# Kernel tuning notes

Measured on AMD Instinct MI355X. Metric: run time of the kernel, lower is better.

The kernel has to match this reference:

```python
import jax, jax.numpy as jnp
import numpy as np

N, E, CIN, H, B, NCOV, NCLASS, T = 50000, 800000, 64, 64, 256, 8, 2, 3


def setup_inputs() -> dict:
    key = jax.random.key(0)
    ks = jax.random.split(key, 24)
    s = 1.0 / np.sqrt(H)
    nrm = lambda k, shp, sc: (jax.random.normal(k, shp, jnp.float32) * sc)
    p = {}
    p["x"] = nrm(ks[0], (N, 3 * CIN), 1.0)
    p["edge_index"] = jax.random.randint(ks[1], (2, E), 0, N)
    p["cov"] = nrm(ks[2], (B, NCOV), 1.0)
    p["batch"] = jnp.sort(jax.random.randint(ks[3], (N,), 0, B))
    p["h0"] = nrm(ks[4], (B, H), 1.0)
    p["c0"] = nrm(ks[5], (B, H), 1.0)
    # GCNEncoder params (shared across the 3 channel slices, as in the torch code)
    p["lin_W"] = nrm(ks[6], (CIN, H), s)
    p["lin_b"] = jnp.zeros((H,), jnp.float32)
    p["conv1_W"] = nrm(ks[7], (H, H), s)
    p["conv1_b"] = jnp.zeros((H,), jnp.float32)
    p["conv2_W"] = nrm(ks[8], (H, H), s)
    p["conv2_b"] = jnp.zeros((H,), jnp.float32)
    # LSTM (1 layer), torch gate order i,f,g,o
    p["Wih"] = nrm(ks[9], (4 * H, H), s)
    p["Whh"] = nrm(ks[10], (4 * H, H), s)
    p["bih"] = jnp.zeros((4 * H,), jnp.float32)
    p["bhh"] = jnp.zeros((4 * H,), jnp.float32)
    p["w0_W"] = nrm(ks[11], (H, H), s)
    p["w0_b"] = jnp.zeros((H,), jnp.float32)
    p["attn_W"] = nrm(ks[12], (1, H), s)
    p["attn_b"] = jnp.zeros((1,), jnp.float32)
    p["l1_W"] = nrm(ks[13], (8, H), s)
    p["l1_b"] = jnp.zeros((8,), jnp.float32)
    p["l2_W"] = nrm(ks[14], (NCLASS, 8 + NCOV), 1.0 / np.sqrt(8 + NCOV))
    p["l2_b"] = jnp.zeros((NCLASS,), jnp.float32)
    return p


def _gcn_conv(x, src, dst, dinv, W, b):
    xw = x @ W
    norm = dinv[src] * dinv[dst]                      # [E]
    agg = jax.ops.segment_sum(norm[:, None] * xw[src], dst, num_segments=N)
    agg = agg + (2.0 * dinv * dinv)[:, None] * xw     # self-loop (weight 2)
    return agg + b


def _encoder(x, src, dst, dinv, lin_W, lin_b, c1W, c1b, c2W, c2b):
    out = x @ lin_W + lin_b                           # dropout = identity (eval)
    out1 = jax.nn.relu(_gcn_conv(out, src, dst, dinv, c1W, c1b)) + out
    out2 = _gcn_conv(out1, src, dst, dinv, c2W, c2b) + out1
    return out2


def reference(x, edge_index, cov, batch, h0, c0, lin_W, lin_b, conv1_W, conv1_b,
              conv2_W, conv2_b, Wih, Whh, bih, bhh, w0_W, w0_b, attn_W, attn_b,
              l1_W, l1_b, l2_W, l2_b):
    src, dst = edge_index[0], edge_index[1]
    deg = jax.ops.segment_sum(jnp.ones((E,), jnp.float32), dst, num_segments=N) + 2.0
    dinv = jax.lax.rsqrt(deg)
    enc = lambda xi: _encoder(xi, src, dst, dinv, lin_W, lin_b,
                              conv1_W, conv1_b, conv2_W, conv2_b)
    o1 = enc(x[:, :CIN]); o2 = enc(x[:, CIN:2 * CIN]); o3 = enc(x[:, 2 * CIN:])
    # global_mean_pool per branch
    cnt = jnp.maximum(jax.ops.segment_sum(jnp.ones((N,), jnp.float32), batch,
                                          num_segments=B), 1.0)[:, None]
    pool = lambda o: jax.ops.segment_sum(o, batch, num_segments=B) / cnt
    seq = jnp.stack([pool(o1), pool(o2), pool(o3)], axis=1)  # [B, 3, H]

    # 1-layer LSTM over T=3 (torch gate order i,f,g,o)
    def step(carry, x_t):
        h, c = carry
        g = x_t @ Wih.T + bih + h @ Whh.T + bhh
        i, f, gg, o = jnp.split(g, 4, axis=-1)
        c = jax.nn.sigmoid(f) * c + jax.nn.sigmoid(i) * jnp.tanh(gg)
        h = jax.nn.sigmoid(o) * jnp.tanh(c)
        return (h, c), h

    (_, _), hs = jax.lax.scan(step, (h0, c0), jnp.swapaxes(seq, 0, 1))
    rnn_out = jnp.swapaxes(hs, 0, 1)                         # [B, T, H]
    r = jnp.tanh(rnn_out @ w0_W.T + w0_b)
    attn = jax.nn.softmax((r @ attn_W.T + attn_b)[..., 0], axis=1)  # [B, T]
    pooled = jnp.einsum('bth,bt->bh', r, attn)
    out = jax.nn.relu(pooled @ l1_W.T + l1_b)
    out = jnp.concatenate([out, cov], axis=1)
    out = out @ l2_W.T + l2_b
    return attn, out
```

## Files before the change

kernel.cpp:

```cpp
#include <hip/hip_runtime.h>
#include <math.h>


#define TT 3
#define CHUNK 2048

typedef __attribute__((ext_vector_type(2))) float floatx2;

__device__ __forceinline__ float sigmoidf_(float x) { return 1.f / (1.f + expf(-x)); }

__global__ void brow_sorted(const int* __restrict__ batch, int* __restrict__ brow,
                            int N, int B) {
    int n = blockIdx.x * 256 + threadIdx.x;
    if (n >= N) return;
    int b = batch[n];
    if (n == 0) {
        for (int q = 0; q <= b; ++q) brow[q] = 0;
    } else {
        int pb = batch[n - 1];
        for (int q = pb + 1; q <= b; ++q) brow[q] = n;
    }
    if (n == N - 1) {
        for (int q = b + 1; q <= B; ++q) brow[q] = N;
    }
}

__global__ void hist_kernel(const int* __restrict__ dst, int* __restrict__ bcnt, int E) {
    __shared__ int h[256];
    h[threadIdx.x] = 0;
    __syncthreads();
    int base = blockIdx.x * CHUNK;
    for (int i = threadIdx.x; i < CHUNK; i += 256) {
        int e = base + i;
        if (e < E) atomicAdd(&h[dst[e] >> 8], 1);
    }
    __syncthreads();
    int v = h[threadIdx.x];
    if (v) atomicAdd(&bcnt[threadIdx.x], v);
}

__global__ void scan_buckets(const int* __restrict__ bcnt, int* __restrict__ boff,
                             int* __restrict__ bcur, int nb, int E) {
    __shared__ int s[256];
    int v = (threadIdx.x < nb) ? bcnt[threadIdx.x] : 0;
    s[threadIdx.x] = v;
    __syncthreads();
    for (int off = 1; off < 256; off <<= 1) {
        int t = (threadIdx.x >= off) ? s[threadIdx.x - off] : 0;
        __syncthreads();
        s[threadIdx.x] += t;
        __syncthreads();
    }
    if (threadIdx.x < nb) { boff[threadIdx.x] = s[threadIdx.x] - v; bcur[threadIdx.x] = s[threadIdx.x] - v; }
    if (threadIdx.x == 0) boff[nb] = E;
}

__global__ void stage_kernel(const int* __restrict__ src, const int* __restrict__ dst,
                             int* __restrict__ bcur, unsigned* __restrict__ stg, int E) {
    __shared__ int hcnt[256], hbase[256], hcur[256];
    hcnt[threadIdx.x] = 0;
    __syncthreads();
    int base = blockIdx.x * CHUNK;
    for (int i = threadIdx.x; i < CHUNK; i += 256) {
        int e = base + i;
        if (e < E) atomicAdd(&hcnt[dst[e] >> 8], 1);
    }
    __syncthreads();
    int c = hcnt[threadIdx.x];
    if (c) hbase[threadIdx.x] = atomicAdd(&bcur[threadIdx.x], c);
    hcur[threadIdx.x] = 0;
    __syncthreads();
    for (int i = threadIdx.x; i < CHUNK; i += 256) {
        int e = base + i;
        if (e < E) {
            int d = dst[e];
            int b = d >> 8;
            int r = atomicAdd(&hcur[b], 1);
            stg[hbase[b] + r] = (unsigned)src[e] | ((unsigned)(d & 255) << 24);
        }
    }
}

__global__ void bucket_build(const unsigned* __restrict__ stg, const int* __restrict__ boff,
                             int* __restrict__ rowptr, float* __restrict__ dinv,
                             int* __restrict__ csrc, int N, int E) {
    const int b = blockIdx.x;
    const int n0 = b << 8;
    __shared__ int cnt[256];
    __shared__ int pfx[256];
    cnt[threadIdx.x] = 0;
    __syncthreads();
    const int s = boff[b], e = boff[b + 1];
    for (int p = s + threadIdx.x; p < e; p += 256)
        atomicAdd(&cnt[stg[p] >> 24], 1);
    __syncthreads();
    int v = cnt[threadIdx.x];
    pfx[threadIdx.x] = v;
    __syncthreads();
    for (int off = 1; off < 256; off <<= 1) {
        int t = (threadIdx.x >= off) ? pfx[threadIdx.x - off] : 0;
        __syncthreads();
        pfx[threadIdx.x] += t;
        __syncthreads();
    }
    int rowbase = s + pfx[threadIdx.x] - v;
    int n = n0 + threadIdx.x;
    if (n < N) {
        rowptr[n] = rowbase;
        dinv[n] = rsqrtf((float)v + 2.0f);
    }
    if (b == 0 && threadIdx.x == 0) rowptr[N] = E;
    cnt[threadIdx.x] = rowbase;
    __syncthreads();
    for (int p = s + threadIdx.x; p < e; p += 256) {
        unsigned u = stg[p];
        int dl = u >> 24;
        int r = atomicAdd(&cnt[dl], 1);
        csrc[r] = (int)(u & 0xFFFFFFu);
    }
}

__global__ __launch_bounds__(256) void gemm64_v2(
    const float* __restrict__ A, int lda, long aStride,
    const float* __restrict__ W, const float* __restrict__ bias,
    float* __restrict__ C, long cStride,
    unsigned* __restrict__ T8, const float* __restrict__ dinvp, int nrows) {
    __shared__ float AT[64][68];
    __shared__ float Ws[64][68];
    const int t = threadIdx.x;
    const float* Ab = A + (long)blockIdx.y * aStride;
    const int r0 = blockIdx.x * 64;

    #pragma unroll
    for (int i = 0; i < 4; ++i) {
        int idx = t + i * 256;
        int k = idx >> 4, c4 = idx & 15;
        float4 w = *(const float4*)(W + k * 64 + c4 * 4);
        *(float4*)&Ws[k][c4 * 4] = w;
    }
    #pragma unroll
    for (int i = 0; i < 4; ++i) {
        int idx = t + i * 256;
        int row = idx >> 4, c4 = idx & 15;
        int gr = r0 + row;
        float4 a = make_float4(0.f, 0.f, 0.f, 0.f);
        if (gr < nrows) a = *(const float4*)(Ab + (long)gr * lda + c4 * 4);
        AT[c4 * 4 + 0][row] = a.x;
        AT[c4 * 4 + 1][row] = a.y;
        AT[c4 * 4 + 2][row] = a.z;
        AT[c4 * 4 + 3][row] = a.w;
    }
    __syncthreads();

    const int rowg = t >> 4;
    const int colg = t & 15;
    float acc[4][4] = {};
    #pragma unroll 8
    for (int k = 0; k < 64; ++k) {
        float4 av = *(const float4*)&AT[k][rowg * 4];
        float4 wv = *(const float4*)&Ws[k][colg * 4];
        acc[0][0] = fmaf(av.x, wv.x, acc[0][0]);
        acc[0][1] = fmaf(av.x, wv.y, acc[0][1]);
        acc[0][2] = fmaf(av.x, wv.z, acc[0][2]);
        acc[0][3] = fmaf(av.x, wv.w, acc[0][3]);
        acc[1][0] = fmaf(av.y, wv.x, acc[1][0]);
        acc[1][1] = fmaf(av.y, wv.y, acc[1][1]);
        acc[1][2] = fmaf(av.y, wv.z, acc[1][2]);
        acc[1][3] = fmaf(av.y, wv.w, acc[1][3]);
        acc[2][0] = fmaf(av.z, wv.x, acc[2][0]);
        acc[2][1] = fmaf(av.z, wv.y, acc[2][1]);
        acc[2][2] = fmaf(av.z, wv.z, acc[2][2]);
        acc[2][3] = fmaf(av.z, wv.w, acc[2][3]);
        acc[3][0] = fmaf(av.w, wv.x, acc[3][0]);
        acc[3][1] = fmaf(av.w, wv.y, acc[3][1]);
        acc[3][2] = fmaf(av.w, wv.z, acc[3][2]);
        acc[3][3] = fmaf(av.w, wv.w, acc[3][3]);
    }

    float b0 = bias ? bias[colg * 4 + 0] : 0.f;
    float b1 = bias ? bias[colg * 4 + 1] : 0.f;
    float b2 = bias ? bias[colg * 4 + 2] : 0.f;
    float b3 = bias ? bias[colg * 4 + 3] : 0.f;
    #pragma unroll
    for (int i = 0; i < 4; ++i) {
        int gr = r0 + rowg * 4 + i;
        if (gr >= nrows) continue;
        float c0 = acc[i][0] + b0, c1 = acc[i][1] + b1;
        float c2 = acc[i][2] + b2, c3 = acc[i][3] + b3;
        if (C) {
            float* Cb = C + (long)blockIdx.y * cStride;
            *(float4*)(Cb + (long)gr * 64 + colg * 4) = make_float4(c0, c1, c2, c3);
        }
        if (T8) {
            float sc = dinvp[gr];
            int r = 0;
            r = __builtin_amdgcn_cvt_pk_fp8_f32(c0 * sc, c1 * sc, r, false);
            r = __builtin_amdgcn_cvt_pk_fp8_f32(c2 * sc, c3 * sc, r, true);
            T8[(long)gr * 48 + blockIdx.y * 16 + colg] = (unsigned)r;
        }
    }
}

template <bool RELU>
__global__ __launch_bounds__(256) void gcn_gather3_f8(
    const int* __restrict__ rowptr, const int* __restrict__ csrc,
    const float* __restrict__ dinv, const unsigned* __restrict__ tc,
    const float* __restrict__ bias, const float* __restrict__ prev, long chS,
    float* __restrict__ outp, int N) {
    long gid = ((long)blockIdx.x * 256 + threadIdx.x) >> 4;
    int n = (int)gid;
    if (n >= N) return;
    const int jj = threadIdx.x & 15;

    const int end = rowptr[n + 1];
    const float din = dinv[n];
    float a0[TT] = {}, a1[TT] = {}, a2[TT] = {}, a3[TT] = {};
    int p = rowptr[n];
    for (; p + 3 < end; p += 4) {
        long r0 = (long)csrc[p] * 48 + jj;
        long r1 = (long)csrc[p + 1] * 48 + jj;
        long r2 = (long)csrc[p + 2] * 48 + jj;
        long r3 = (long)csrc[p + 3] * 48 + jj;
        #pragma unroll
        for (int ch = 0; ch < TT; ++ch) {
            unsigned u0 = tc[r0 + ch * 16];
            unsigned u1 = tc[r1 + ch * 16];
            unsigned u2 = tc[r2 + ch * 16];
            unsigned u3 = tc[r3 + ch * 16];
            floatx2 l0 = __builtin_amdgcn_cvt_pk_f32_fp8(u0, false);
            floatx2 h0 = __builtin_amdgcn_cvt_pk_f32_fp8(u0, true);
            floatx2 l1 = __builtin_amdgcn_cvt_pk_f32_fp8(u1, false);
            floatx2 h1 = __builtin_amdgcn_cvt_pk_f32_fp8(u1, true);
            floatx2 l2 = __builtin_amdgcn_cvt_pk_f32_fp8(u2, false);
            floatx2 h2 = __builtin_amdgcn_cvt_pk_f32_fp8(u2, true);
            floatx2 l3 = __builtin_amdgcn_cvt_pk_f32_fp8(u3, false);
            floatx2 h3 = __builtin_amdgcn_cvt_pk_f32_fp8(u3, true);
            a0[ch] += (l0.x + l1.x) + (l2.x + l3.x);
            a1[ch] += (l0.y + l1.y) + (l2.y + l3.y);
            a2[ch] += (h0.x + h1.x) + (h2.x + h3.x);
            a3[ch] += (h0.y + h1.y) + (h2.y + h3.y);
        }
    }
    for (; p < end; ++p) {
        long r = (long)csrc[p] * 48 + jj;
        #pragma unroll
        for (int ch = 0; ch < TT; ++ch) {
            unsigned u = tc[r + ch * 16];
            floatx2 lo = __builtin_amdgcn_cvt_pk_f32_fp8(u, false);
            floatx2 hi = __builtin_amdgcn_cvt_pk_f32_fp8(u, true);
            a0[ch] += lo.x; a1[ch] += lo.y; a2[ch] += hi.x; a3[ch] += hi.y;
        }
    }
    float4 bv = *(const float4*)(bias + 4 * jj);
    long nrow = (long)n * 48 + jj;
    long off = (long)n * 64 + 4 * jj;
    #pragma unroll
    for (int ch = 0; ch < TT; ++ch) {
        unsigned us = tc[nrow + ch * 16];
        floatx2 slo = __builtin_amdgcn_cvt_pk_f32_fp8(us, false);
        floatx2 shi = __builtin_amdgcn_cvt_pk_f32_fp8(us, true);
        float v0 = (a0[ch] + 2.f * slo.x) * din + bv.x;
        float v1 = (a1[ch] + 2.f * slo.y) * din + bv.y;
        float v2 = (a2[ch] + 2.f * shi.x) * din + bv.z;
        float v3 = (a3[ch] + 2.f * shi.y) * din + bv.w;
        if (RELU) {
            v0 = fmaxf(v0, 0.f); v1 = fmaxf(v1, 0.f);
            v2 = fmaxf(v2, 0.f); v3 = fmaxf(v3, 0.f);
        }
        float4 pv = *(const float4*)(prev + ch * chS + off);
        *(float4*)(outp + ch * chS + off) =
            make_float4(v0 + pv.x, v1 + pv.y, v2 + pv.z, v3 + pv.w);
    }
}

__global__ __launch_bounds__(256) void pool_range(
    const float* __restrict__ out2, long chStride, const int* __restrict__ brow,
    float* __restrict__ seq) {
    const int b = blockIdx.x;
    const int chan = blockIdx.y;
    const float* src = out2 + (long)chan * chStride;
    const int j = threadIdx.x & 63;
    const int w = threadIdx.x >> 6;
    __shared__ float part[4][64];
    float acc = 0.f;
    const int s = brow[b], e = brow[b + 1];
    for (int n = s + w; n < e; n += 4) acc += src[(long)n * 64 + j];
    part[w][j] = acc;
    __syncthreads();
    if (w == 0)
        seq[((long)b * TT + chan) * 64 + j] = part[0][j] + part[1][j] + part[2][j] + part[3][j];
}

__global__ __launch_bounds__(256) void head_kernel(
    const float* __restrict__ seq, const int* __restrict__ brow,
    const float* __restrict__ h0, const float* __restrict__ c0,
    const float* __restrict__ Wih, const float* __restrict__ Whh,
    const float* __restrict__ bih, const float* __restrict__ bhh,
    const float* __restrict__ w0W, const float* __restrict__ w0b,
    const float* __restrict__ attnW, const float* __restrict__ attnb,
    const float* __restrict__ l1W, const float* __restrict__ l1b,
    const float* __restrict__ l2W, const float* __restrict__ l2b,
    const float* __restrict__ cov, float* __restrict__ out_attn,
    float* __restrict__ out_cls) {
    const int b = blockIdx.x;
    const int t = threadIdx.x;

    __shared__ float x[TT][64];
    __shared__ float h[64], c[64];
    __shared__ float gates[256];
    __shared__ float rnn[TT][64];
    __shared__ float r[TT][64];
    __shared__ float logit[TT];
    __shared__ float a[TT];
    __shared__ float pooled[64];
    __shared__ float l1o[16];

    float inv = 1.0f / fmaxf((float)(brow[b + 1] - brow[b]), 1.0f);
    if (t < TT * 64) x[t / 64][t % 64] = seq[(long)b * TT * 64 + t] * inv;
    if (t < 64) { h[t] = h0[(long)b * 64 + t]; c[t] = c0[(long)b * 64 + t]; }
    __syncthreads();

    for (int step = 0; step < TT; ++step) {
        float g = bih[t] + bhh[t];
        const float* wi = Wih + (long)t * 64;
        const float* wh = Whh + (long)t * 64;
        #pragma unroll 8
        for (int k = 0; k < 64; ++k) g += wi[k] * x[step][k] + wh[k] * h[k];
        gates[t] = g;
        __syncthreads();
        if (t < 64) {
            float ig = sigmoidf_(gates[t]);
            float fg = sigmoidf_(gates[64 + t]);
            float gg = tanhf(gates[128 + t]);
            float og = sigmoidf_(gates[192 + t]);
            float cn = fg * c[t] + ig * gg;
            c[t] = cn;
            float hn = og * tanhf(cn);
            h[t] = hn;
            rnn[step][t] = hn;
        }
        __syncthreads();
    }

    if (t < TT * 64) {
        int tt = t / 64, j = t % 64;
        float v = w0b[j];
        const float* wr = w0W + (long)j * 64;
        #pragma unroll 8
        for (int k = 0; k < 64; ++k) v += rnn[tt][k] * wr[k];
        r[tt][j] = tanhf(v);
    }
    __syncthreads();

    if (t < TT) {
        float v = attnb[0];
        #pragma unroll 8
        for (int k = 0; k < 64; ++k) v += r[t][k] * attnW[k];
        logit[t] = v;
    }
    __syncthreads();

    if (t == 0) {
        float m = fmaxf(logit[0], fmaxf(logit[1], logit[2]));
        float e0 = expf(logit[0] - m), e1 = expf(logit[1] - m), e2 = expf(logit[2] - m);
        float s = e0 + e1 + e2;
        a[0] = e0 / s; a[1] = e1 / s; a[2] = e2 / s;
        out_attn[(long)b * TT + 0] = a[0];
        out_attn[(long)b * TT + 1] = a[1];
        out_attn[(long)b * TT + 2] = a[2];
    }
    __syncthreads();

    if (t < 64) pooled[t] = a[0] * r[0][t] + a[1] * r[1][t] + a[2] * r[2][t];
    __syncthreads();

    if (t < 8) {
        float v = l1b[t];
        const float* w = l1W + (long)t * 64;
        #pragma unroll 8
        for (int k = 0; k < 64; ++k) v += pooled[k] * w[k];
        l1o[t] = fmaxf(v, 0.f);
    } else if (t < 16) {
        l1o[t] = cov[(long)b * 8 + (t - 8)];
    }
    __syncthreads();

    if (t < 2) {
        float v = l2b[t];
        const float* w = l2W + (long)t * 16;
        #pragma unroll
        for (int k = 0; k < 16; ++k) v += l1o[k] * w[k];
        out_cls[(long)b * 2 + t] = v;
    }
}

extern "C" void kernel_launch(void* const* d_in, const int* in_sizes, int n_in,
                              void* d_out, int out_size, void* d_ws, size_t ws_size,
                              hipStream_t stream) {
    const float* x       = (const float*)d_in[0];
    const int*   eidx    = (const int*)d_in[1];
    const float* cov     = (const float*)d_in[2];
    const int*   batch   = (const int*)d_in[3];
    const float* h0      = (const float*)d_in[4];
    const float* c0      = (const float*)d_in[5];
    const float* lin_W   = (const float*)d_in[6];
    const float* lin_b   = (const float*)d_in[7];
    const float* conv1_W = (const float*)d_in[8];
    const float* conv1_b = (const float*)d_in[9];
    const float* conv2_W = (const float*)d_in[10];
    const float* conv2_b = (const float*)d_in[11];
    const float* Wih     = (const float*)d_in[12];
    const float* Whh     = (const float*)d_in[13];
    const float* bih     = (const float*)d_in[14];
    const float* bhh     = (const float*)d_in[15];
    const float* w0_W    = (const float*)d_in[16];
    const float* w0_b    = (const float*)d_in[17];
    const float* attn_W  = (const float*)d_in[18];
    const float* attn_b  = (const float*)d_in[19];
    const float* l1_W    = (const float*)d_in[20];
    const float* l1_b    = (const float*)d_in[21];
    const float* l2_W    = (const float*)d_in[22];
    const float* l2_b    = (const float*)d_in[23];

    const int N = in_sizes[3];
    const int E = in_sizes[1] / 2;
    const int B = in_sizes[2] / 8;

    const int* src = eidx;
    const int* dst = eidx + E;

    auto cdiv = [](long a, long b) { return (int)((a + b - 1) / b); };
    const int nb = cdiv(N, 256);

    char* w = (char*)d_ws;
    float* dinv   = (float*)w;  w += (size_t)N * 4;
    int*   rowptr = (int*)w;    w += (size_t)(N + 1) * 4;
    int*   brow   = (int*)w;    w += (size_t)(B + 1) * 4;
    int*   bcnt   = (int*)w;    w += 256 * 4;
    int*   boff   = (int*)w;    w += 260 * 4;
    int*   bcur   = (int*)w;    w += 256 * 4;
    int*   csrc   = (int*)w;    w += (size_t)E * 4;
    unsigned* stg = (unsigned*)w; w += (size_t)E * 4;
    float* seq    = (float*)w;  w += (size_t)B * TT * 64 * 4;
    float* buf0   = (float*)w;  w += (size_t)TT * N * 64 * 4;
    float* bufA   = (float*)w;  w += (size_t)TT * N * 64 * 4;
    unsigned* tb8 = (unsigned*)w;  w += (size_t)N * 48 * 4;
    const long chS = (long)N * 64;

    float* out_attn = (float*)d_out;
    float* out_cls  = out_attn + (long)B * TT;

    hipMemsetAsync(bcnt, 0, 256 * 4, stream);
    brow_sorted<<<cdiv(N, 256), 256, 0, stream>>>(batch, brow, N, B);
    hist_kernel<<<cdiv(E, CHUNK), 256, 0, stream>>>(dst, bcnt, E);
    scan_buckets<<<1, 256, 0, stream>>>(bcnt, boff, bcur, nb, E);
    stage_kernel<<<cdiv(E, CHUNK), 256, 0, stream>>>(src, dst, bcur, stg, E);
    bucket_build<<<nb, 256, 0, stream>>>(stg, boff, rowptr, dinv, csrc, N, E);

    const int gemm_gx = cdiv(N, 64);
    const int ng_gx   = cdiv((long)N * 16, 256);

    {
        dim3 ggrid(gemm_gx, TT);
        gemm64_v2<<<ggrid, 256, 0, stream>>>(x, 3 * 64, 64, lin_W, lin_b,
                                             buf0, chS, nullptr, nullptr, N);
    }
    {
        dim3 ggrid(gemm_gx, TT);
        gemm64_v2<<<ggrid, 256, 0, stream>>>(buf0, 64, chS, conv1_W, nullptr,
                                             nullptr, 0, tb8, dinv, N);
    }
    gcn_gather3_f8<true><<<ng_gx, 256, 0, stream>>>(
        rowptr, csrc, dinv, tb8, conv1_b, buf0, chS, bufA, N);
    {
        dim3 ggrid(gemm_gx, TT);
        gemm64_v2<<<ggrid, 256, 0, stream>>>(bufA, 64, chS, conv2_W, nullptr,
                                             nullptr, 0, tb8, dinv, N);
    }
    gcn_gather3_f8<false><<<ng_gx, 256, 0, stream>>>(
        rowptr, csrc, dinv, tb8, conv2_b, bufA, chS, buf0, N);

    {
        dim3 pgrid(B, TT);
        pool_range<<<pgrid, 256, 0, stream>>>(buf0, chS, brow, seq);
    }

    head_kernel<<<B, 256, 0, stream>>>(seq, brow, h0, c0, Wih, Whh, bih, bhh,
                                       w0_W, w0_b, attn_W, attn_b, l1_W, l1_b,
                                       l2_W, l2_b, cov, out_attn, out_cls);
}
```

Baseline: 256.0 us.

## Fuse lin and conv1 GEMMs, drop histogram pass, unroll gather by eight

Fuses the input linear layer and the conv1 GEMM into one kernel that keeps the intermediate tile in shared memory. The fused kernel still writes buf0 for the residual path and no longer re-reads it for the second GEMM. The CSR build drops its separate histogram pass by staging edges into fixed-capacity per-bucket slots (BCAP) and scanning the counts afterwards. This assumes no bucket of 256 destination nodes holds more than 16384 edges. The gather loop is unrolled to eight edges per iteration to raise memory-level parallelism, at some register cost.

```diff
diff --git a/kernel.cpp b/kernel.cpp
--- a/kernel.cpp
+++ b/kernel.cpp
@@ -4,6 +4,7 @@
 
 #define TT 3
 #define CHUNK 2048
+#define BCAP 16384
 
 typedef __attribute__((ext_vector_type(2))) float floatx2;
 
@@ -25,38 +26,8 @@
     }
 }
 
-__global__ void hist_kernel(const int* __restrict__ dst, int* __restrict__ bcnt, int E) {
-    __shared__ int h[256];
-    h[threadIdx.x] = 0;
-    __syncthreads();
-    int base = blockIdx.x * CHUNK;
-    for (int i = threadIdx.x; i < CHUNK; i += 256) {
-        int e = base + i;
-        if (e < E) atomicAdd(&h[dst[e] >> 8], 1);
-    }
-    __syncthreads();
-    int v = h[threadIdx.x];
-    if (v) atomicAdd(&bcnt[threadIdx.x], v);
-}
-
-__global__ void scan_buckets(const int* __restrict__ bcnt, int* __restrict__ boff,
-                             int* __restrict__ bcur, int nb, int E) {
-    __shared__ int s[256];
-    int v = (threadIdx.x < nb) ? bcnt[threadIdx.x] : 0;
-    s[threadIdx.x] = v;
-    __syncthreads();
-    for (int off = 1; off < 256; off <<= 1) {
-        int t = (threadIdx.x >= off) ? s[threadIdx.x - off] : 0;
-        __syncthreads();
-        s[threadIdx.x] += t;
-        __syncthreads();
-    }
-    if (threadIdx.x < nb) { boff[threadIdx.x] = s[threadIdx.x] - v; bcur[threadIdx.x] = s[threadIdx.x] - v; }
-    if (threadIdx.x == 0) boff[nb] = E;
-}
-
-__global__ void stage_kernel(const int* __restrict__ src, const int* __restrict__ dst,
-                             int* __restrict__ bcur, unsigned* __restrict__ stg, int E) {
+__global__ void stage_direct(const int* __restrict__ src, const int* __restrict__ dst,
+                             int* __restrict__ bcnt, unsigned* __restrict__ stg, int E) {
     __shared__ int hcnt[256], hbase[256], hcur[256];
     hcnt[threadIdx.x] = 0;
     __syncthreads();
@@ -67,7 +38,7 @@
     }
     __syncthreads();
     int c = hcnt[threadIdx.x];
-    if (c) hbase[threadIdx.x] = atomicAdd(&bcur[threadIdx.x], c);
+    if (c) hbase[threadIdx.x] = atomicAdd(&bcnt[threadIdx.x], c);
     hcur[threadIdx.x] = 0;
     __syncthreads();
     for (int i = threadIdx.x; i < CHUNK; i += 256) {
@@ -76,22 +47,41 @@
             int d = dst[e];
             int b = d >> 8;
             int r = atomicAdd(&hcur[b], 1);
-            stg[hbase[b] + r] = (unsigned)src[e] | ((unsigned)(d & 255) << 24);
-        }
-    }
-}
-
-__global__ void bucket_build(const unsigned* __restrict__ stg, const int* __restrict__ boff,
-                             int* __restrict__ rowptr, float* __restrict__ dinv,
-                             int* __restrict__ csrc, int N, int E) {
+            stg[(long)b * BCAP + hbase[b] + r] =
+                (unsigned)src[e] | ((unsigned)(d & 255) << 24);
+        }
+    }
+}
+
+__global__ void scan_buckets(const int* __restrict__ bcnt, int* __restrict__ boff,
+                             int nb, int E) {
+    __shared__ int s[256];
+    int v = (threadIdx.x < nb) ? bcnt[threadIdx.x] : 0;
+    s[threadIdx.x] = v;
+    __syncthreads();
+    for (int off = 1; off < 256; off <<= 1) {
+        int t = (threadIdx.x >= off) ? s[threadIdx.x - off] : 0;
+        __syncthreads();
+        s[threadIdx.x] += t;
+        __syncthreads();
+    }
+    if (threadIdx.x < nb) boff[threadIdx.x] = s[threadIdx.x] - v;
+    if (threadIdx.x == 0) boff[nb] = E;
+}
+
+__global__ void bucket_build(const unsigned* __restrict__ stg, const int* __restrict__ bcnt,
+                             const int* __restrict__ boff, int* __restrict__ rowptr,
+                             float* __restrict__ dinv, int* __restrict__ csrc,
+                             int N, int E) {
     const int b = blockIdx.x;
     const int n0 = b << 8;
     __shared__ int cnt[256];
     __shared__ int pfx[256];
     cnt[threadIdx.x] = 0;
     __syncthreads();
-    const int s = boff[b], e = boff[b + 1];
-    for (int p = s + threadIdx.x; p < e; p += 256)
+    const long s = (long)b * BCAP;
+    const long e = s + bcnt[b];
+    for (long p = s + threadIdx.x; p < e; p += 256)
         atomicAdd(&cnt[stg[p] >> 24], 1);
     __syncthreads();
     int v = cnt[threadIdx.x];
@@ -103,7 +93,7 @@
         pfx[threadIdx.x] += t;
         __syncthreads();
     }
-    int rowbase = s + pfx[threadIdx.x] - v;
+    int rowbase = boff[b] + pfx[threadIdx.x] - v;
     int n = n0 + threadIdx.x;
     if (n < N) {
         rowptr[n] = rowbase;
@@ -112,7 +102,7 @@
     if (b == 0 && threadIdx.x == 0) rowptr[N] = E;
     cnt[threadIdx.x] = rowbase;
     __syncthreads();
-    for (int p = s + threadIdx.x; p < e; p += 256) {
+    for (long p = s + threadIdx.x; p < e; p += 256) {
         unsigned u = stg[p];
         int dl = u >> 24;
         int r = atomicAdd(&cnt[dl], 1);
@@ -120,10 +110,102 @@
     }
 }
 
-__global__ __launch_bounds__(256) void gemm64_v2(
-    const float* __restrict__ A, int lda, long aStride,
-    const float* __restrict__ W, const float* __restrict__ bias,
-    float* __restrict__ C, long cStride,
+__global__ __launch_bounds__(256) void gemm_lin_conv1(
+    const float* __restrict__ x, const float* __restrict__ W1,
+    const float* __restrict__ b1, const float* __restrict__ W2,
+    float* __restrict__ buf0, long chS,
+    unsigned* __restrict__ T8, const float* __restrict__ dinvp, int nrows) {
+    __shared__ float AT[64][68];
+    __shared__ float Ws[64][68];
+    const int t = threadIdx.x;
+    const int r0 = blockIdx.x * 64;
+    const int rowg = t >> 4, colg = t & 15;
+
+    #pragma unroll
+    for (int i = 0; i < 4; ++i) {
+        int idx = t + i * 256;
+        int k = idx >> 4, c4 = idx & 15;
+        *(float4*)&Ws[k][c4 * 4] = *(const float4*)(W1 + k * 64 + c4 * 4);
+    }
+    #pragma unroll
+    for (int i = 0; i < 4; ++i) {
+        int idx = t + i * 256;
+        int row = idx >> 4, c4 = idx & 15;
+        int gr = r0 + row;
+        float4 a = make_float4(0.f, 0.f, 0.f, 0.f);
+        if (gr < nrows) a = *(const float4*)(x + (long)gr * 192 + blockIdx.y * 64 + c4 * 4);
+        AT[c4 * 4 + 0][row] = a.x;
+        AT[c4 * 4 + 1][row] = a.y;
+        AT[c4 * 4 + 2][row] = a.z;
+        AT[c4 * 4 + 3][row] = a.w;
+    }
+    __syncthreads();
+
+    float acc[4][4] = {};
+    #pragma unroll 8
+    for (int k = 0; k < 64; ++k) {
+        float4 av = *(const float4*)&AT[k][rowg * 4];
+        float4 wv = *(const float4*)&Ws[k][colg * 4];
+        #pragma unroll
+        for (int i = 0; i < 4; ++i) {
+            acc[i][0] = fmaf(((const float*)&av)[i], wv.x, acc[i][0]);
+            acc[i][1] = fmaf(((const float*)&av)[i], wv.y, acc[i][1]);
+            acc[i][2] = fmaf(((const float*)&av)[i], wv.z, acc[i][2]);
+            acc[i][3] = fmaf(((const float*)&av)[i], wv.w, acc[i][3]);
+        }
+    }
+    float b_0 = b1[colg * 4 + 0], b_1 = b1[colg * 4 + 1];
+    float b_2 = b1[colg * 4 + 2], b_3 = b1[colg * 4 + 3];
+    __syncthreads();
+    float* buf0c = buf0 + (long)blockIdx.y * chS;
+    #pragma unroll
+    for (int i = 0; i < 4; ++i) {
+        int gr = r0 + rowg * 4 + i;
+        float c0 = acc[i][0] + b_0, c1 = acc[i][1] + b_1;
+        float c2 = acc[i][2] + b_2, c3 = acc[i][3] + b_3;
+        if (gr < nrows)
+            *(float4*)(buf0c + (long)gr * 64 + colg * 4) = make_float4(c0, c1, c2, c3);
+        int row = rowg * 4 + i;
+        AT[colg * 4 + 0][row] = c0;
+        AT[colg * 4 + 1][row] = c1;
+        AT[colg * 4 + 2][row] = c2;
+        AT[colg * 4 + 3][row] = c3;
+    }
+    #pragma unroll
+    for (int i = 0; i < 4; ++i) {
+        int idx = t + i * 256;
+        int k = idx >> 4, c4 = idx & 15;
+        *(float4*)&Ws[k][c4 * 4] = *(const float4*)(W2 + k * 64 + c4 * 4);
+    }
+    __syncthreads();
+
+    float acc2[4][4] = {};
+    #pragma unroll 8
+    for (int k = 0; k < 64; ++k) {
+        float4 av = *(const float4*)&AT[k][rowg * 4];
+        float4 wv = *(const float4*)&Ws[k][colg * 4];
+        #pragma unroll
+        for (int i = 0; i < 4; ++i) {
+            acc2[i][0] = fmaf(((const float*)&av)[i], wv.x, acc2[i][0]);
+            acc2[i][1] = fmaf(((const float*)&av)[i], wv.y, acc2[i][1]);
+            acc2[i][2] = fmaf(((const float*)&av)[i], wv.z, acc2[i][2]);
+            acc2[i][3] = fmaf(((const float*)&av)[i], wv.w, acc2[i][3]);
+        }
+    }
+    #pragma unroll
+    for (int i = 0; i < 4; ++i) {
+        int gr = r0 + rowg * 4 + i;
+        if (gr >= nrows) continue;
+        float sc = dinvp[gr];
+        int r = 0;
+        r = __builtin_amdgcn_cvt_pk_fp8_f32(acc2[i][0] * sc, acc2[i][1] * sc, r, false);
+        r = __builtin_amdgcn_cvt_pk_fp8_f32(acc2[i][2] * sc, acc2[i][3] * sc, r, true);
+        T8[(long)gr * 48 + blockIdx.y * 16 + colg] = (unsigned)r;
+    }
+}
+
+__global__ __launch_bounds__(256) void gemm64_t8(
+    const float* __restrict__ A, long aStride, const float* __restrict__ W,
     unsigned* __restrict__ T8, const float* __restrict__ dinvp, int nrows) {
     __shared__ float AT[64][68];
     __shared__ float Ws[64][68];
@@ -135,8 +217,7 @@
     for (int i = 0; i < 4; ++i) {
         int idx = t + i * 256;
         int k = idx >> 4, c4 = idx & 15;
-        float4 w = *(const float4*)(W + k * 64 + c4 * 4);
-        *(float4*)&Ws[k][c4 * 4] = w;
+        *(float4*)&Ws[k][c4 * 4] = *(const float4*)(W + k * 64 + c4 * 4);
     }
     #pragma unroll
     for (int i = 0; i < 4; ++i) {
@@ -144,7 +225,7 @@
         int row = idx >> 4, c4 = idx & 15;
         int gr = r0 + row;
         float4 a = make_float4(0.f, 0.f, 0.f, 0.f);
-        if (gr < nrows) a = *(const float4*)(Ab + (long)gr * lda + c4 * 4);
+        if (gr < nrows) a = *(const float4*)(Ab + (long)gr * 64 + c4 * 4);
         AT[c4 * 4 + 0][row] = a.x;
         AT[c4 * 4 + 1][row] = a.y;
         AT[c4 * 4 + 2][row] = a.z;
@@ -152,54 +233,38 @@
     }
     __syncthreads();
 
-    const int rowg = t >> 4;
-    const int colg = t & 15;
+    const int rowg = t >> 4, colg = t & 15;
     float acc[4][4] = {};
     #pragma unroll 8
     for (int k = 0; k < 64; ++k) {
         float4 av = *(const float4*)&AT[k][rowg * 4];
         float4 wv = *(const float4*)&Ws[k][colg * 4];
-        acc[0][0] = fmaf(av.x, wv.x, acc[0][0]);
-        acc[0][1] = fmaf(av.x, wv.y, acc[0][1]);
-        acc[0][2] = fmaf(av.x, wv.z, acc[0][2]);
-        acc[0][3] = fmaf(av.x, wv.w, acc[0][3]);
-        acc[1][0] = fmaf(av.y, wv.x, acc[1][0]);
-        acc[1][1] = fmaf(av.y, wv.y, acc[1][1]);
-        acc[1][2] = fmaf(av.y, wv.z, acc[1][2]);
-        acc[1][3] = fmaf(av.y, wv.w, acc[1][3]);
-        acc[2][0] = fmaf(av.z, wv.x, acc[2][0]);
-        acc[2][1] = fmaf(av.z, wv.y, acc[2][1]);
-        acc[2][2] = fmaf(av.z, wv.z, acc[2][2]);
-        acc[2][3] = fmaf(av.z, wv.w, acc[2][3]);
-        acc[3][0] = fmaf(av.w, wv.x, acc[3][0]);
-        acc[3][1] = fmaf(av.w, wv.y, acc[3][1]);
-        acc[3][2] = fmaf(av.w, wv.z, acc[3][2]);
-        acc[3][3] = fmaf(av.w, wv.w, acc[3][3]);
-    }
-
-    float b0 = bias ? bias[colg * 4 + 0] : 0.f;
-    float b1 = bias ? bias[colg * 4 + 1] : 0.f;
-    float b2 = bias ? bias[colg * 4 + 2] : 0.f;
-    float b3 = bias ? bias[colg * 4 + 3] : 0.f;
+        #pragma unroll
+        for (int i = 0; i < 4; ++i) {
+            acc[i][0] = fmaf(((const float*)&av)[i], wv.x, acc[i][0]);
+            acc[i][1] = fmaf(((const float*)&av)[i], wv.y, acc[i][1]);
+            acc[i][2] = fmaf(((const float*)&av)[i], wv.z, acc[i][2]);
+            acc[i][3] = fmaf(((const float*)&av)[i], wv.w, acc[i][3]);
+        }
+    }
     #pragma unroll
     for (int i = 0; i < 4; ++i) {
         int gr = r0 + rowg * 4 + i;
         if (gr >= nrows) continue;
-        float c0 = acc[i][0] + b0, c1 = acc[i][1] + b1;
-        float c2 = acc[i][2] + b2, c3 = acc[i][3] + b3;
-        if (C) {
-            float* Cb = C + (long)blockIdx.y * cStride;
-            *(float4*)(Cb + (long)gr * 64 + colg * 4) = make_float4(c0, c1, c2, c3);
-        }
-        if (T8) {
-            float sc = dinvp[gr];
-            int r = 0;
-            r = __builtin_amdgcn_cvt_pk_fp8_f32(c0 * sc, c1 * sc, r, false);
-            r = __builtin_amdgcn_cvt_pk_fp8_f32(c2 * sc, c3 * sc, r, true);
-            T8[(long)gr * 48 + blockIdx.y * 16 + colg] = (unsigned)r;
-        }
-    }
-}
+        float sc = dinvp[gr];
+        int r = 0;
+        r = __builtin_amdgcn_cvt_pk_fp8_f32(acc[i][0] * sc, acc[i][1] * sc, r, false);
+        r = __builtin_amdgcn_cvt_pk_fp8_f32(acc[i][2] * sc, acc[i][3] * sc, r, true);
+        T8[(long)gr * 48 + blockIdx.y * 16 + colg] = (unsigned)r;
+    }
+}
+
+#define EDGE3(uu)                                                        \
+    {                                                                    \
+        floatx2 lo = __builtin_amdgcn_cvt_pk_f32_fp8(uu, false);         \
+        floatx2 hi = __builtin_amdgcn_cvt_pk_f32_fp8(uu, true);          \
+        a0[ch] += lo.x; a1[ch] += lo.y; a2[ch] += hi.x; a3[ch] += hi.y;  \
+    }
 
 template <bool RELU>
 __global__ __launch_bounds__(256) void gcn_gather3_f8(
@@ -216,29 +281,27 @@
     const float din = dinv[n];
     float a0[TT] = {}, a1[TT] = {}, a2[TT] = {}, a3[TT] = {};
     int p = rowptr[n];
-    for (; p + 3 < end; p += 4) {
-        long r0 = (long)csrc[p] * 48 + jj;
+    for (; p + 7 < end; p += 8) {
+        long r0 = (long)csrc[p]     * 48 + jj;
         long r1 = (long)csrc[p + 1] * 48 + jj;
         long r2 = (long)csrc[p + 2] * 48 + jj;
         long r3 = (long)csrc[p + 3] * 48 + jj;
+        long r4 = (long)csrc[p + 4] * 48 + jj;
+        long r5 = (long)csrc[p + 5] * 48 + jj;
+        long r6 = (long)csrc[p + 6] * 48 + jj;
+        long r7 = (long)csrc[p + 7] * 48 + jj;
         #pragma unroll
         for (int ch = 0; ch < TT; ++ch) {
             unsigned u0 = tc[r0 + ch * 16];
             unsigned u1 = tc[r1 + ch * 16];
             unsigned u2 = tc[r2 + ch * 16];
             unsigned u3 = tc[r3 + ch * 16];
-            floatx2 l0 = __builtin_amdgcn_cvt_pk_f32_fp8(u0, false);
-            floatx2 h0 = __builtin_amdgcn_cvt_pk_f32_fp8(u0, true);
-            floatx2 l1 = __builtin_amdgcn_cvt_pk_f32_fp8(u1, false);
-            floatx2 h1 = __builtin_amdgcn_cvt_pk_f32_fp8(u1, true);
-            floatx2 l2 = __builtin_amdgcn_cvt_pk_f32_fp8(u2, false);
-            floatx2 h2 = __builtin_amdgcn_cvt_pk_f32_fp8(u2, true);
-            floatx2 l3 = __builtin_amdgcn_cvt_pk_f32_fp8(u3, false);
-            floatx2 h3 = __builtin_amdgcn_cvt_pk_f32_fp8(u3, true);
-            a0[ch] += (l0.x + l1.x) + (l2.x + l3.x);
-            a1[ch] += (l0.y + l1.y) + (l2.y + l3.y);
-            a2[ch] += (h0.x + h1.x) + (h2.x + h3.x);
-            a3[ch] += (h0.y + h1.y) + (h2.y + h3.y);
+            unsigned u4 = tc[r4 + ch * 16];
+            unsigned u5 = tc[r5 + ch * 16];
+            unsigned u6 = tc[r6 + ch * 16];
+            unsigned u7 = tc[r7 + ch * 16];
+            EDGE3(u0) EDGE3(u1) EDGE3(u2) EDGE3(u3)
+            EDGE3(u4) EDGE3(u5) EDGE3(u6) EDGE3(u7)
         }
     }
     for (; p < end; ++p) {
@@ -246,9 +309,7 @@
         #pragma unroll
         for (int ch = 0; ch < TT; ++ch) {
             unsigned u = tc[r + ch * 16];
-            floatx2 lo = __builtin_amdgcn_cvt_pk_f32_fp8(u, false);
-            floatx2 hi = __builtin_amdgcn_cvt_pk_f32_fp8(u, true);
-            a0[ch] += lo.x; a1[ch] += lo.y; a2[ch] += hi.x; a3[ch] += hi.y;
+            EDGE3(u)
         }
     }
     float4 bv = *(const float4*)(bias + 4 * jj);
@@ -438,9 +499,8 @@
     int*   brow   = (int*)w;    w += (size_t)(B + 1) * 4;
     int*   bcnt   = (int*)w;    w += 256 * 4;
     int*   boff   = (int*)w;    w += 260 * 4;
-    int*   bcur   = (int*)w;    w += 256 * 4;
     int*   csrc   = (int*)w;    w += (size_t)E * 4;
-    unsigned* stg = (unsigned*)w; w += (size_t)E * 4;
+    unsigned* stg = (unsigned*)w; w += (size_t)nb * BCAP * 4;
     float* seq    = (float*)w;  w += (size_t)B * TT * 64 * 4;
     float* buf0   = (float*)w;  w += (size_t)TT * N * 64 * 4;
     float* bufA   = (float*)w;  w += (size_t)TT * N * 64 * 4;
@@ -452,30 +512,23 @@
 
     hipMemsetAsync(bcnt, 0, 256 * 4, stream);
     brow_sorted<<<cdiv(N, 256), 256, 0, stream>>>(batch, brow, N, B);
-    hist_kernel<<<cdiv(E, CHUNK), 256, 0, stream>>>(dst, bcnt, E);
-    scan_buckets<<<1, 256, 0, stream>>>(bcnt, boff, bcur, nb, E);
-    stage_kernel<<<cdiv(E, CHUNK), 256, 0, stream>>>(src, dst, bcur, stg, E);
-    bucket_build<<<nb, 256, 0, stream>>>(stg, boff, rowptr, dinv, csrc, N, E);
+    stage_direct<<<cdiv(E, CHUNK), 256, 0, stream>>>(src, dst, bcnt, stg, E);
+    scan_buckets<<<1, 256, 0, stream>>>(bcnt, boff, nb, E);
+    bucket_build<<<nb, 256, 0, stream>>>(stg, bcnt, boff, rowptr, dinv, csrc, N, E);
 
     const int gemm_gx = cdiv(N, 64);
     const int ng_gx   = cdiv((long)N * 16, 256);
 
     {
         dim3 ggrid(gemm_gx, TT);
-        gemm64_v2<<<ggrid, 256, 0, stream>>>(x, 3 * 64, 64, lin_W, lin_b,
-                                             buf0, chS, nullptr, nullptr, N);
-    }
-    {
-        dim3 ggrid(gemm_gx, TT);
-        gemm64_v2<<<ggrid, 256, 0, stream>>>(buf0, 64, chS, conv1_W, nullptr,
-                                             nullptr, 0, tb8, dinv, N);
+        gemm_lin_conv1<<<ggrid, 256, 0, stream>>>(x, lin_W, lin_b, conv1_W,
+                                                  buf0, chS, tb8, dinv, N);
     }
     gcn_gather3_f8<true><<<ng_gx, 256, 0, stream>>>(
         rowptr, csrc, dinv, tb8, conv1_b, buf0, chS, bufA, N);
     {
         dim3 ggrid(gemm_gx, TT);
-        gemm64_v2<<<ggrid, 256, 0, stream>>>(bufA, 64, chS, conv2_W, nullptr,
-                                             nullptr, 0, tb8, dinv, N);
+        gemm64_t8<<<ggrid, 256, 0, stream>>>(bufA, chS, conv2_W, tb8, dinv, N);
     }
     gcn_gather3_f8<false><<<ng_gx, 256, 0, stream>>>(
         rowptr, csrc, dinv, tb8, conv2_b, bufA, chS, buf0, N);
```

After: 241.5 us. 5.7% less time.
